# Kernel optimization log

Hardware: AMD Instinct MI355X
Metric: run time of the kernel (lower is better)

The kernel has to match this reference:

```python
import jax, jax.numpy as jnp
import numpy as np

B, L, H, V, HALF = 128, 4096, 64, 64, 32
ALPHA = 0.95
LN_EPS = 1e-5


def _normalize(x):
    # torch F.normalize(dim=-1): x / max(||x||_2, 1e-12)
    n = jnp.linalg.norm(x, axis=-1, keepdims=True)
    return x / jnp.maximum(n, 1e-12)


def setup_inputs() -> dict:
    key = jax.random.key(0)
    ks = jax.random.split(key, 17)
    s = 0.05
    return {
        "seq": jax.random.randint(ks[0], (B, L), 0, V),
        "embed": jax.random.normal(ks[1], (V, H), jnp.float32),
        "W1": jax.random.normal(ks[2], (H, 2 * H), jnp.float32) * s,
        "b1": jnp.zeros((2 * H,), jnp.float32),
        "W2": jax.random.normal(ks[3], (2 * H, H), jnp.float32) * s,
        "b2": jnp.zeros((H,), jnp.float32),
        "gamma": jnp.ones((H,), jnp.float32),
        "beta": jnp.zeros((H,), jnp.float32),
        "Ws": jax.random.normal(ks[4], (H, HALF), jnp.float32) * s,
        "bs": jnp.zeros((HALF,), jnp.float32),
        "We": jax.random.normal(ks[5], (H, HALF), jnp.float32) * s,
        "be": jnp.zeros((HALF,), jnp.float32),
        "Wrp": jax.random.normal(ks[6], (2 * HALF, H), jnp.float32) * s,
        "brp": jnp.zeros((H,), jnp.float32),
        "Wout": jax.random.normal(ks[7], (H, V), jnp.float32) * s,
        "bout": jnp.zeros((V,), jnp.float32),
    }


def _forward(seq, embed, W1, b1, W2, b2, gamma, beta,
             Ws, bs, We, be, Wrp, brp, Wout, bout):
    # Encoder: embed + FF(ReLU) residual + LayerNorm
    h0 = embed[seq]                                   # [B,L,H]
    ff = jnp.maximum(h0 @ W1 + b1, 0.0) @ W2 + b2
    x = h0 + ff
    mu = x.mean(-1, keepdims=True)
    var = ((x - mu) ** 2).mean(-1, keepdims=True)
    h = (x - mu) / jnp.sqrt(var + LN_EPS) * gamma + beta  # [B,L,H]

    # Precompute per-step projections for t = 0 .. L-2
    hp = h[:, :-1, :]                                 # [B,L-1,H]
    hs = hp @ Ws + bs                                 # [B,L-1,HALF]
    he = hp @ We + be
    ksn = _normalize(hs)
    ken = _normalize(he)
    scale = (jnp.arange(L - 1, dtype=h.dtype) + 1.0) / L  # (t+1)/L

    def step(carry, inp):
        M_s, M_e = carry                              # [B,HALF,HALF]
        hs_t, he_t, ks_t, ke_t, sc = inp
        vps = jnp.einsum('bij,bj->bi', M_s, ks_t)
        vpe = jnp.einsum('bij,bj->bi', M_e, ke_t)
        M_s = M_s + (1.0 - ALPHA) * (hs_t - vps)[:, :, None] * ks_t[:, None, :]
        M_e = M_e + (1.0 - ALPHA) * sc * (he_t - vpe)[:, :, None] * ke_t[:, None, :]
        return (M_s, M_e), None

    xs = (jnp.swapaxes(hs, 0, 1), jnp.swapaxes(he, 0, 1),
          jnp.swapaxes(ksn, 0, 1), jnp.swapaxes(ken, 0, 1), scale)
    M0 = jnp.zeros((B, HALF, HALF), h.dtype)
    (M_s, M_e), _ = jax.lax.scan(step, (M0, M0), xs)

    # Read with last-token query
    q = h[:, -1, :]
    qs = _normalize(q @ Ws + bs)
    qe = _normalize(q @ We + be)
    rs = jnp.einsum('bij,bj->bi', M_s, qs)
    re = jnp.einsum('bij,bj->bi', M_e, qe)
    r = jnp.concatenate([rs, re], axis=-1)            # [B,2*HALF]
    return (r @ Wrp + brp) @ Wout + bout              # [B,V]


def reference(seq, embed, W1, b1, W2, b2, gamma, beta,
              Ws, bs, We, be, Wrp, brp, Wout, bout):
    return _forward(seq, embed, W1, b1, W2, b2, gamma, beta,
                    Ws, bs, We, be, Wrp, brp, Wout, bout)
```

## Files before the change

kernel.cpp:

```cpp
#include <hip/hip_runtime.h>
#include <hip/hip_bf16.h>
#include <stdint.h>


#define BETA 0.05f
#define NB 128
#define NL 4096
#define TC 16
#define NCH 256
#define NBLD 6
#define SLOT_F 336
#define NSLOT 12

#define L_GR   (NSLOT * SLOT_F)
#define L_DA   (L_GR + 4096)
#define L_RV   (L_DA + 64)
#define L_O1   (L_RV + 64)
#define L_WHO  (L_O1 + 64)
#define L_TOT  (L_WHO + 1)

struct Ptrs { const void* p[15]; };

__device__ inline float readlane_f(float v, int l) {
    return __int_as_float(__builtin_amdgcn_readlane(__float_as_int(v), l));
}
__device__ inline float ldT(const float* p, int i) { return p[i]; }
__device__ inline float ldT(const __hip_bfloat16* p, int i) { return __bfloat162float(p[i]); }

template <typename T>
__device__ void build_tables_body(const T* emb, const T* W1, const T* b1,
                                  const T* W2, const T* b2, const T* gam,
                                  const T* bet, const T* Wsm, const T* bsv,
                                  const T* Wem, const T* bev, float* tbl)
{
    int v = blockIdx.x;
    int j = threadIdx.x;
    __shared__ float h0s[64];
    __shared__ float act[128];
    __shared__ float hrow[64];

    float h0 = ldT(emb, v * 64 + j);
    h0s[j] = h0;
    __syncthreads();

    float za = ldT(b1, j);
    float zb = ldT(b1, j + 64);
    for (int k = 0; k < 64; ++k) {
        float hk = h0s[k];
        za = fmaf(hk, ldT(W1, k * 128 + j), za);
        zb = fmaf(hk, ldT(W1, k * 128 + j + 64), zb);
    }
    act[j] = fmaxf(za, 0.0f);
    act[j + 64] = fmaxf(zb, 0.0f);
    __syncthreads();

    float ff = ldT(b2, j);
    for (int k = 0; k < 128; ++k)
        ff = fmaf(act[k], ldT(W2, k * 64 + j), ff);
    float x = h0 + ff;

    float s = x;
    for (int off = 32; off >= 1; off >>= 1) s += __shfl_xor(s, off, 64);
    float mu = s * (1.0f / 64.0f);
    float d = x - mu;
    float s2 = d * d;
    for (int off = 32; off >= 1; off >>= 1) s2 += __shfl_xor(s2, off, 64);
    float var = s2 * (1.0f / 64.0f);
    float h = d / sqrtf(var + 1e-5f) * ldT(gam, j) + ldT(bet, j);
    hrow[j] = h;
    __syncthreads();

    if (j < 32) {
        float sv = ldT(bsv, j);
        for (int k = 0; k < 64; ++k)
            sv = fmaf(hrow[k], ldT(Wsm, k * 32 + j), sv);
        float n2 = sv * sv;
        for (int off = 16; off >= 1; off >>= 1) n2 += __shfl_xor(n2, off, 64);
        float nrm = fmaxf(sqrtf(n2), 1e-12f);
        tbl[v * 32 + j] = sv;
        tbl[2048 + v * 32 + j] = sv / nrm;
    } else {
        int jj = j - 32;
        float ev = ldT(bev, jj);
        for (int k = 0; k < 64; ++k)
            ev = fmaf(hrow[k], ldT(Wem, k * 32 + jj), ev);
        float n2 = ev * ev;
        for (int off = 16; off >= 1; off >>= 1) n2 += __shfl_xor(n2, off, 64);
        float nrm = fmaxf(sqrtf(n2), 1e-12f);
        tbl[4096 + v * 32 + jj] = ev;
        tbl[6144 + v * 32 + jj] = ev / nrm;
    }
}

__global__ __launch_bounds__(64, 2) void build_tables(Ptrs ps, float* __restrict__ tbl,
                                                      int* __restrict__ flags)
{
    if (blockIdx.x == 0) {
        flags[threadIdx.x] = 0;
        flags[threadIdx.x + 64] = 0;
    }
    uint32_t g0 = *(const uint32_t*)ps.p[5];
    if (g0 == 0x3F803F80u)
        build_tables_body((const __hip_bfloat16*)ps.p[0], (const __hip_bfloat16*)ps.p[1],
                          (const __hip_bfloat16*)ps.p[2], (const __hip_bfloat16*)ps.p[3],
                          (const __hip_bfloat16*)ps.p[4], (const __hip_bfloat16*)ps.p[5],
                          (const __hip_bfloat16*)ps.p[6], (const __hip_bfloat16*)ps.p[7],
                          (const __hip_bfloat16*)ps.p[8], (const __hip_bfloat16*)ps.p[9],
                          (const __hip_bfloat16*)ps.p[10], tbl);
    else
        build_tables_body((const float*)ps.p[0], (const float*)ps.p[1],
                          (const float*)ps.p[2], (const float*)ps.p[3],
                          (const float*)ps.p[4], (const float*)ps.p[5],
                          (const float*)ps.p[6], (const float*)ps.p[7],
                          (const float*)ps.p[8], (const float*)ps.p[9],
                          (const float*)ps.p[10], tbl);
}

__global__ __launch_bounds__(512, 1) void ema_ms(
    const int* __restrict__ seq, const float* __restrict__ tbl,
    Ptrs ps, float* __restrict__ rvbuf, int* __restrict__ flags,
    void* __restrict__ outv)
{
    __shared__ __align__(16) float S[L_TOT];

    int bm = blockIdx.x;
    int b = bm >> 1, mat = bm & 1;
    int tid = threadIdx.x;
    int wid = tid >> 6, lane = tid & 63;
    const float bstep = BETA / 4096.0f;

    if (tid < 64) S[L_DA + tid] = 0.0f;

    const float* ktab = tbl + 2048 + mat * 4096;
    for (int i = tid; i < 2048; i += 512)
        S[(i >> 5) * 33 + (i & 31)] = ktab[i];
    __syncthreads();

    {
        float Kown[32];
#pragma unroll
        for (int j = 0; j < 32; ++j) Kown[j] = S[lane * 33 + j];
        for (int v8 = 0; v8 < 8; ++v8) {
            int vt = wid * 8 + v8;
            float acc = 0.0f;
#pragma unroll
            for (int j = 0; j < 32; ++j)
                acc = fmaf(S[vt * 33 + j], Kown[j], acc);
            S[L_GR + vt * 64 + lane] = acc;
        }
    }
    __syncthreads();

    const int* sb = seq + (size_t)b * NL;
    float y = 0.0f;
    if (wid == 0) {
        int vlast = sb[NL - 1];
        y = S[L_GR + vlast * 64 + lane];
    }

    const int NRND = (NCH + NBLD - 1) / NBLD;

    for (int r = 0; r <= NRND; ++r) {
        if (wid != 0 && wid != 4) {
            int bi = (wid > 4) ? (wid - 2) : (wid - 1);
            int ci = NBLD * r + bi;
            if (r < NRND && ci < NCH) {
                int c = NCH - 1 - ci;
                float* slot = S + ((r & 1) * NBLD + bi) * SLOT_F;
                int tokv = 0; float bneg = 0.0f;
                if (lane < TC) {
                    int t = c * TC + (TC - 1) - lane;
                    tokv = sb[t];
                    float bb = mat ? bstep * (float)(t + 1) : BETA;
                    if (t == NL - 1) bb = 0.0f;
                    bneg = -bb;
                    ((int*)(slot + 320))[lane] = tokv;
                }
                float garr[TC];
#pragma unroll
                for (int p = 0; p < TC; ++p) {
                    int vp = __builtin_amdgcn_readlane(tokv, p);
                    garr[p] = S[L_GR + vp * 64 + tokv] * bneg;
                }
                float z[TC];
                z[15] = (lane == 15) ? 1.0f : 0.0f;
#pragma unroll
                for (int q = TC - 2; q >= 0; --q) {
                    float zq = (lane == q) ? 1.0f : 0.0f;
#pragma unroll
                    for (int j2 = q + 1; j2 < TC; ++j2)
                        zq = fmaf(readlane_f(garr[j2], q), z[j2], zq);
                    z[q] = zq;
                }
                if (lane < TC) {
                    float4* vd = (float4*)(slot + lane * 20);
                    vd[0] = make_float4(z[0], z[1], z[2], z[3]);
                    vd[1] = make_float4(z[4], z[5], z[6], z[7]);
                    vd[2] = make_float4(z[8], z[9], z[10], z[11]);
                    vd[3] = make_float4(z[12], z[13], z[14], z[15]);
                }
            }
        } else if (wid == 0 && r >= 1) {
            int rpar = ((r - 1) & 1) * NBLD;
            int base_ci = NBLD * (r - 1);
            int nch_r = NCH - base_ci;
            if (nch_r > NBLD) nch_r = NBLD;
            int l15 = lane & 15;

            int tokr[NBLD];
#pragma unroll
            for (int j = 0; j < NBLD; ++j)
                tokr[j] = ((int*)(S + (rpar + j) * SLOT_F + 320))[l15];

            int stok[2][16];
            float gp[2][16];
            float4 V[2][4];
#pragma unroll
            for (int j = 0; j < 2; ++j) {
#pragma unroll
                for (int q = 0; q < 16; ++q)
                    stok[j][q] = __builtin_amdgcn_readlane(tokr[j], q);
                const float4* vr = (const float4*)(S + (rpar + j) * SLOT_F + l15 * 20);
#pragma unroll
                for (int k = 0; k < 4; ++k) V[j][k] = vr[k];
#pragma unroll
                for (int p = 0; p < 16; ++p)
                    gp[j][p] = S[L_GR + stok[j][p] * 64 + lane];
            }
            asm volatile("" ::: "memory");

#pragma unroll
            for (int jj = 0; jj < NBLD; ++jj) {
                const int pb = jj & 1;
                if (jj < nch_r) {
                    int c = NCH - 1 - (base_ci + jj);
                    float bv = 0.0f;
                    if (lane < TC) {
                        int t = c * TC + (TC - 1) - lane;
                        float bb = mat ? bstep * (float)(t + 1) : BETA;
                        if (t == NL - 1) bb = 0.0f;
                        bv = bb;
                    }
                    float ryq[16];
#pragma unroll
                    for (int q = 0; q < 16; ++q)
                        ryq[q] = readlane_f(y, stok[pb][q]);
                    float s0 = V[pb][0].x * ryq[0];
                    float s1 = V[pb][0].y * ryq[1];
                    float s2 = V[pb][0].z * ryq[2];
                    float s3 = V[pb][0].w * ryq[3];
                    s0 = fmaf(V[pb][1].x, ryq[4], s0);
                    s1 = fmaf(V[pb][1].y, ryq[5], s1);
                    s2 = fmaf(V[pb][1].z, ryq[6], s2);
                    s3 = fmaf(V[pb][1].w, ryq[7], s3);
                    s0 = fmaf(V[pb][2].x, ryq[8], s0);
                    s1 = fmaf(V[pb][2].y, ryq[9], s1);
                    s2 = fmaf(V[pb][2].z, ryq[10], s2);
                    s3 = fmaf(V[pb][2].w, ryq[11], s3);
                    s0 = fmaf(V[pb][3].x, ryq[12], s0);
                    s1 = fmaf(V[pb][3].y, ryq[13], s1);
                    s2 = fmaf(V[pb][3].z, ryq[14], s2);
                    s3 = fmaf(V[pb][3].w, ryq[15], s3);
                    float dv = ((s0 + s1) + (s2 + s3)) * bv;
                    float dn = -dv;
                    float ya = 0.f, yb = 0.f, yc2 = 0.f, yd = 0.f;
#pragma unroll
                    for (int p = 0; p < TC; p += 4) {
                        ya  = fmaf(readlane_f(dn, p),     gp[pb][p],     ya);
                        yb  = fmaf(readlane_f(dn, p + 1), gp[pb][p + 1], yb);
                        yc2 = fmaf(readlane_f(dn, p + 2), gp[pb][p + 2], yc2);
                        yd  = fmaf(readlane_f(dn, p + 3), gp[pb][p + 3], yd);
                    }
                    y += (ya + yb) + (yc2 + yd);
                    if (lane < TC) atomicAdd(&S[L_DA + tokr[jj]], dv);
                }
                if (jj + 2 < NBLD) {
                    const int j2 = jj + 2;
#pragma unroll
                    for (int q = 0; q < 16; ++q)
                        stok[pb][q] = __builtin_amdgcn_readlane(tokr[j2], q);
                    const float4* vr = (const float4*)(S + (rpar + j2) * SLOT_F + l15 * 20);
#pragma unroll
                    for (int k = 0; k < 4; ++k) V[pb][k] = vr[k];
#pragma unroll
                    for (int p = 0; p < 16; ++p)
                        gp[pb][p] = S[L_GR + stok[pb][p] * 64 + lane];
                }
                asm volatile("" ::: "memory");
            }
        }
        __syncthreads();
    }

    if (tid < 32) {
        float rr = 0.0f;
        const float* hsrc = tbl + mat * 4096;
        for (int v = 0; v < 64; ++v)
            rr = fmaf(S[L_DA + v], hsrc[v * 32 + tid], rr);
        __hip_atomic_store(&rvbuf[bm * 32 + tid], rr,
                           __ATOMIC_RELAXED, __HIP_MEMORY_SCOPE_AGENT);
    }
    __syncthreads();
    if (tid == 0) {
        int old = __hip_atomic_fetch_add(&flags[b], 1,
                                         __ATOMIC_ACQ_REL, __HIP_MEMORY_SCOPE_AGENT);
        ((int*)S)[L_WHO] = old;
    }
    __syncthreads();
    if (((int*)S)[L_WHO] != 1) return;

    if (tid < 64)
        S[L_RV + tid] = __hip_atomic_load(&rvbuf[b * 64 + tid],
                                          __ATOMIC_RELAXED, __HIP_MEMORY_SCOPE_AGENT);
    __syncthreads();

    uint32_t g0h = *(const uint32_t*)ps.p[5];
    int isbf = (g0h == 0x3F803F80u) ? 1 : 0;
    if (tid < 64) {
        float o;
        if (isbf) {
            const __hip_bfloat16* W = (const __hip_bfloat16*)ps.p[11];
            o = __bfloat162float(((const __hip_bfloat16*)ps.p[12])[tid]);
            for (int i = 0; i < 64; ++i)
                o = fmaf(S[L_RV + i], __bfloat162float(W[i * 64 + tid]), o);
        } else {
            const float* W = (const float*)ps.p[11];
            o = ((const float*)ps.p[12])[tid];
            for (int i = 0; i < 64; ++i)
                o = fmaf(S[L_RV + i], W[i * 64 + tid], o);
        }
        S[L_O1 + tid] = o;
    }
    __syncthreads();
    if (tid < 64) {
        float o2;
        if (isbf) {
            const __hip_bfloat16* W = (const __hip_bfloat16*)ps.p[13];
            o2 = __bfloat162float(((const __hip_bfloat16*)ps.p[14])[tid]);
            for (int i = 0; i < 64; ++i)
                o2 = fmaf(S[L_O1 + i], __bfloat162float(W[i * 64 + tid]), o2);
            ((__hip_bfloat16*)outv)[b * 64 + tid] = __float2bfloat16(o2);
        } else {
            const float* W = (const float*)ps.p[13];
            o2 = ((const float*)ps.p[14])[tid];
            for (int i = 0; i < 64; ++i)
                o2 = fmaf(S[L_O1 + i], W[i * 64 + tid], o2);
            ((float*)outv)[b * 64 + tid] = o2;
        }
    }
}

extern "C" void kernel_launch(void* const* d_in, const int* in_sizes, int n_in,
                              void* d_out, int out_size, void* d_ws, size_t ws_size,
                              hipStream_t stream) {
    const int* seq = (const int*)d_in[0];
    Ptrs ps;
    for (int i = 0; i < 15; ++i) ps.p[i] = d_in[i + 1];

    float* tbl = (float*)d_ws;
    float* rvbuf = tbl + 8192;
    int* flags = (int*)(rvbuf + 8192);

    build_tables<<<64, 64, 0, stream>>>(ps, tbl, flags);
    ema_ms<<<NB * 2, 512, 0, stream>>>(seq, tbl, ps, rvbuf, flags, d_out);
}
```

Measured before the change: 191.2 us.

## Build four chunk tables per builder wave and enlarge rounds to cut barriers

Each builder wave now packs four 16-lane groups, each solving one chunk's triangular system with a forward-substitution recast using width-16 shuffles. A round therefore covers 24 chunks instead of 6, and the slot buffer grows to 48. This reduces the number of block-wide barrier rounds and uses all 64 lanes of each builder wave instead of 16. In exchange it costs more LDS, more serial work per round for the consumer wave, and shuffle-based cross-lane reads in place of readlane.

```diff
diff --git a/kernel.cpp b/kernel.cpp
--- a/kernel.cpp
+++ b/kernel.cpp
@@ -9,8 +9,9 @@
 #define TC 16
 #define NCH 256
 #define NBLD 6
+#define RCH 24
 #define SLOT_F 336
-#define NSLOT 12
+#define NSLOT 48
 
 #define L_GR   (NSLOT * SLOT_F)
 #define L_DA   (L_GR + 4096)
@@ -158,58 +159,62 @@
         y = S[L_GR + vlast * 64 + lane];
     }
 
-    const int NRND = (NCH + NBLD - 1) / NBLD;
+    const int NRND = (NCH + RCH - 1) / RCH;
 
     for (int r = 0; r <= NRND; ++r) {
         if (wid != 0 && wid != 4) {
             int bi = (wid > 4) ? (wid - 2) : (wid - 1);
-            int ci = NBLD * r + bi;
-            if (r < NRND && ci < NCH) {
-                int c = NCH - 1 - ci;
-                float* slot = S + ((r & 1) * NBLD + bi) * SLOT_F;
-                int tokv = 0; float bneg = 0.0f;
-                if (lane < TC) {
-                    int t = c * TC + (TC - 1) - lane;
-                    tokv = sb[t];
-                    float bb = mat ? bstep * (float)(t + 1) : BETA;
-                    if (t == NL - 1) bb = 0.0f;
-                    bneg = -bb;
-                    ((int*)(slot + 320))[lane] = tokv;
-                }
+            if (r < NRND) {
+                int g = lane >> 4, q = lane & 15;
+                int ci = RCH * r + 4 * bi + g;
+                int valid = (ci < NCH);
+                int cic = valid ? ci : (NCH - 1);
+                int c = NCH - 1 - cic;
+                float* slot = S + ((r & 1) * RCH + 4 * bi + g) * SLOT_F;
+                int t = c * TC + (TC - 1) - q;
+                int tokv = sb[t];
+                float bb = mat ? bstep * (float)(t + 1) : BETA;
+                if (t == NL - 1) bb = 0.0f;
+                float bneg = -bb;
+                if (valid) ((int*)(slot + 320))[q] = tokv;
+
                 float garr[TC];
 #pragma unroll
                 for (int p = 0; p < TC; ++p) {
-                    int vp = __builtin_amdgcn_readlane(tokv, p);
+                    int vp = __shfl(tokv, p, 16);
                     garr[p] = S[L_GR + vp * 64 + tokv] * bneg;
                 }
-                float z[TC];
-                z[15] = (lane == 15) ? 1.0f : 0.0f;
-#pragma unroll
-                for (int q = TC - 2; q >= 0; --q) {
-                    float zq = (lane == q) ? 1.0f : 0.0f;
-#pragma unroll
-                    for (int j2 = q + 1; j2 < TC; ++j2)
-                        zq = fmaf(readlane_f(garr[j2], q), z[j2], zq);
-                    z[q] = zq;
-                }
-                if (lane < TC) {
-                    float4* vd = (float4*)(slot + lane * 20);
-                    vd[0] = make_float4(z[0], z[1], z[2], z[3]);
-                    vd[1] = make_float4(z[4], z[5], z[6], z[7]);
-                    vd[2] = make_float4(z[8], z[9], z[10], z[11]);
-                    vd[3] = make_float4(z[12], z[13], z[14], z[15]);
+                float x[TC];
+                x[0] = (q == 0) ? 1.0f : 0.0f;
+#pragma unroll
+                for (int p = 1; p < TC; ++p) {
+                    float t0 = 0.f, t1 = 0.f, t2 = 0.f, t3 = 0.f;
+#pragma unroll
+                    for (int j2 = 0; j2 < p; ++j2) {
+                        float cpj = __shfl(garr[p], j2, 16);
+                        if ((j2 & 3) == 0)      t0 = fmaf(cpj, x[j2], t0);
+                        else if ((j2 & 3) == 1) t1 = fmaf(cpj, x[j2], t1);
+                        else if ((j2 & 3) == 2) t2 = fmaf(cpj, x[j2], t2);
+                        else                    t3 = fmaf(cpj, x[j2], t3);
+                    }
+                    x[p] = ((q == p) ? 1.0f : 0.0f) + ((t0 + t1) + (t2 + t3));
+                }
+                if (valid) {
+#pragma unroll
+                    for (int p = 0; p < TC; ++p)
+                        slot[p * 20 + q] = x[p];
                 }
             }
         } else if (wid == 0 && r >= 1) {
-            int rpar = ((r - 1) & 1) * NBLD;
-            int base_ci = NBLD * (r - 1);
+            int rpar = ((r - 1) & 1) * RCH;
+            int base_ci = RCH * (r - 1);
             int nch_r = NCH - base_ci;
-            if (nch_r > NBLD) nch_r = NBLD;
+            if (nch_r > RCH) nch_r = RCH;
             int l15 = lane & 15;
 
-            int tokr[NBLD];
-#pragma unroll
-            for (int j = 0; j < NBLD; ++j)
+            int tokr[RCH];
+#pragma unroll
+            for (int j = 0; j < RCH; ++j)
                 tokr[j] = ((int*)(S + (rpar + j) * SLOT_F + 320))[l15];
 
             int stok[2][16];
@@ -230,7 +235,7 @@
             asm volatile("" ::: "memory");
 
 #pragma unroll
-            for (int jj = 0; jj < NBLD; ++jj) {
+            for (int jj = 0; jj < RCH; ++jj) {
                 const int pb = jj & 1;
                 if (jj < nch_r) {
                     int c = NCH - 1 - (base_ci + jj);
@@ -274,7 +279,7 @@
                     y += (ya + yb) + (yc2 + yd);
                     if (lane < TC) atomicAdd(&S[L_DA + tokr[jj]], dv);
                 }
-                if (jj + 2 < NBLD) {
+                if (jj + 2 < RCH) {
                     const int j2 = jj + 2;
 #pragma unroll
                     for (int q = 0; q < 16; ++q)
```

Result: no change. 189.0 us (-1.1%).

## Precompute per-chunk combined W matrix in builder waves to shorten serial scan

Applied to the files above, without the earlier changes.

Builder waves now do more per chunk. They compute the forward triangular solve with beta folded in, then precompute a 64x16 matrix W = X^T·(beta·G) and store it in enlarged LDS slots. The serial wave 0 no longer gathers G rows or runs the dependent readlane reduction over dv; it does two independent 16-term dot products per chunk, one for the y update and one for the accumulated delta. The sign is fixed at the end by negating rr. This moves work off the critical serial path in exchange for more LDS per slot and more builder-side arithmetic.

```diff
diff --git a/kernel.cpp b/kernel.cpp
--- a/kernel.cpp
+++ b/kernel.cpp
@@ -9,7 +9,7 @@
 #define TC 16
 #define NCH 256
 #define NBLD 6
-#define SLOT_F 336
+#define SLOT_F 1616
 #define NSLOT 12
 
 #define L_GR   (NSLOT * SLOT_F)
@@ -174,30 +174,57 @@
                     float bb = mat ? bstep * (float)(t + 1) : BETA;
                     if (t == NL - 1) bb = 0.0f;
                     bneg = -bb;
-                    ((int*)(slot + 320))[lane] = tokv;
-                }
-                float garr[TC];
+                    ((int*)(slot + 1600))[lane] = tokv;
+                }
+                float garr[TC], gp[TC];
 #pragma unroll
                 for (int p = 0; p < TC; ++p) {
                     int vp = __builtin_amdgcn_readlane(tokv, p);
                     garr[p] = S[L_GR + vp * 64 + tokv] * bneg;
-                }
-                float z[TC];
-                z[15] = (lane == 15) ? 1.0f : 0.0f;
-#pragma unroll
-                for (int q = TC - 2; q >= 0; --q) {
-                    float zq = (lane == q) ? 1.0f : 0.0f;
-#pragma unroll
-                    for (int j2 = q + 1; j2 < TC; ++j2)
-                        zq = fmaf(readlane_f(garr[j2], q), z[j2], zq);
-                    z[q] = zq;
+                    gp[p]   = S[L_GR + vp * 64 + lane];
+                }
+                float x[TC];
+                x[0] = (lane == 0) ? 1.0f : 0.0f;
+#pragma unroll
+                for (int p = 1; p < TC; ++p) {
+                    float t0 = 0.f, t1 = 0.f, t2 = 0.f, t3 = 0.f;
+#pragma unroll
+                    for (int j2 = 0; j2 < p; ++j2) {
+                        float cpj = readlane_f(garr[p], j2);
+                        if ((j2 & 3) == 0)      t0 = fmaf(cpj, x[j2], t0);
+                        else if ((j2 & 3) == 1) t1 = fmaf(cpj, x[j2], t1);
+                        else if ((j2 & 3) == 2) t2 = fmaf(cpj, x[j2], t2);
+                        else                    t3 = fmaf(cpj, x[j2], t3);
+                    }
+                    x[p] = ((lane == p) ? 1.0f : 0.0f) + ((t0 + t1) + (t2 + t3));
                 }
                 if (lane < TC) {
-                    float4* vd = (float4*)(slot + lane * 20);
-                    vd[0] = make_float4(z[0], z[1], z[2], z[3]);
-                    vd[1] = make_float4(z[4], z[5], z[6], z[7]);
-                    vd[2] = make_float4(z[8], z[9], z[10], z[11]);
-                    vd[3] = make_float4(z[12], z[13], z[14], z[15]);
+#pragma unroll
+                    for (int p = 0; p < TC; ++p)
+                        slot[p * 20 + lane] = x[p] * readlane_f(bneg, p);
+                }
+                float gpb[TC];
+#pragma unroll
+                for (int p = 0; p < TC; ++p)
+                    gpb[p] = gp[p] * readlane_f(bneg, p);
+                float4* wd = (float4*)(slot + 320 + lane * 20);
+#pragma unroll
+                for (int q4 = 0; q4 < 4; ++q4) {
+                    float w[4];
+#pragma unroll
+                    for (int qi = 0; qi < 4; ++qi) {
+                        const int q = 4 * q4 + qi;
+                        float a0 = 0.f, a1 = 0.f, a2 = 0.f, a3 = 0.f;
+#pragma unroll
+                        for (int p = 0; p < TC; p += 4) {
+                            a0 = fmaf(readlane_f(x[p],     q), gpb[p],     a0);
+                            a1 = fmaf(readlane_f(x[p + 1], q), gpb[p + 1], a1);
+                            a2 = fmaf(readlane_f(x[p + 2], q), gpb[p + 2], a2);
+                            a3 = fmaf(readlane_f(x[p + 3], q), gpb[p + 3], a3);
+                        }
+                        w[qi] = (a0 + a1) + (a2 + a3);
+                    }
+                    wd[q4] = make_float4(w[0], w[1], w[2], w[3]);
                 }
             }
         } else if (wid == 0 && r >= 1) {
@@ -210,22 +237,22 @@
             int tokr[NBLD];
 #pragma unroll
             for (int j = 0; j < NBLD; ++j)
-                tokr[j] = ((int*)(S + (rpar + j) * SLOT_F + 320))[l15];
+                tokr[j] = ((int*)(S + (rpar + j) * SLOT_F + 1600))[l15];
 
             int stok[2][16];
-            float gp[2][16];
-            float4 V[2][4];
+            float4 W4[2][4];
+            float4 V4[2][4];
 #pragma unroll
             for (int j = 0; j < 2; ++j) {
 #pragma unroll
                 for (int q = 0; q < 16; ++q)
                     stok[j][q] = __builtin_amdgcn_readlane(tokr[j], q);
+                const float4* wr = (const float4*)(S + (rpar + j) * SLOT_F + 320 + lane * 20);
+#pragma unroll
+                for (int k = 0; k < 4; ++k) W4[j][k] = wr[k];
                 const float4* vr = (const float4*)(S + (rpar + j) * SLOT_F + l15 * 20);
 #pragma unroll
-                for (int k = 0; k < 4; ++k) V[j][k] = vr[k];
-#pragma unroll
-                for (int p = 0; p < 16; ++p)
-                    gp[j][p] = S[L_GR + stok[j][p] * 64 + lane];
+                for (int k = 0; k < 4; ++k) V4[j][k] = vr[k];
             }
             asm volatile("" ::: "memory");
 
@@ -233,58 +260,47 @@
             for (int jj = 0; jj < NBLD; ++jj) {
                 const int pb = jj & 1;
                 if (jj < nch_r) {
-                    int c = NCH - 1 - (base_ci + jj);
-                    float bv = 0.0f;
-                    if (lane < TC) {
-                        int t = c * TC + (TC - 1) - lane;
-                        float bb = mat ? bstep * (float)(t + 1) : BETA;
-                        if (t == NL - 1) bb = 0.0f;
-                        bv = bb;
-                    }
                     float ryq[16];
 #pragma unroll
                     for (int q = 0; q < 16; ++q)
                         ryq[q] = readlane_f(y, stok[pb][q]);
-                    float s0 = V[pb][0].x * ryq[0];
-                    float s1 = V[pb][0].y * ryq[1];
-                    float s2 = V[pb][0].z * ryq[2];
-                    float s3 = V[pb][0].w * ryq[3];
-                    s0 = fmaf(V[pb][1].x, ryq[4], s0);
-                    s1 = fmaf(V[pb][1].y, ryq[5], s1);
-                    s2 = fmaf(V[pb][1].z, ryq[6], s2);
-                    s3 = fmaf(V[pb][1].w, ryq[7], s3);
-                    s0 = fmaf(V[pb][2].x, ryq[8], s0);
-                    s1 = fmaf(V[pb][2].y, ryq[9], s1);
-                    s2 = fmaf(V[pb][2].z, ryq[10], s2);
-                    s3 = fmaf(V[pb][2].w, ryq[11], s3);
-                    s0 = fmaf(V[pb][3].x, ryq[12], s0);
-                    s1 = fmaf(V[pb][3].y, ryq[13], s1);
-                    s2 = fmaf(V[pb][3].z, ryq[14], s2);
-                    s3 = fmaf(V[pb][3].w, ryq[15], s3);
-                    float dv = ((s0 + s1) + (s2 + s3)) * bv;
-                    float dn = -dv;
-                    float ya = 0.f, yb = 0.f, yc2 = 0.f, yd = 0.f;
-#pragma unroll
-                    for (int p = 0; p < TC; p += 4) {
-                        ya  = fmaf(readlane_f(dn, p),     gp[pb][p],     ya);
-                        yb  = fmaf(readlane_f(dn, p + 1), gp[pb][p + 1], yb);
-                        yc2 = fmaf(readlane_f(dn, p + 2), gp[pb][p + 2], yc2);
-                        yd  = fmaf(readlane_f(dn, p + 3), gp[pb][p + 3], yd);
+                    float ya = W4[pb][0].x * ryq[0];
+                    float yb = W4[pb][0].y * ryq[1];
+                    float yc2 = W4[pb][0].z * ryq[2];
+                    float yd = W4[pb][0].w * ryq[3];
+#pragma unroll
+                    for (int k = 1; k < 4; ++k) {
+                        ya  = fmaf(W4[pb][k].x, ryq[4 * k + 0], ya);
+                        yb  = fmaf(W4[pb][k].y, ryq[4 * k + 1], yb);
+                        yc2 = fmaf(W4[pb][k].z, ryq[4 * k + 2], yc2);
+                        yd  = fmaf(W4[pb][k].w, ryq[4 * k + 3], yd);
                     }
                     y += (ya + yb) + (yc2 + yd);
-                    if (lane < TC) atomicAdd(&S[L_DA + tokr[jj]], dv);
+                    float s0 = V4[pb][0].x * ryq[0];
+                    float s1 = V4[pb][0].y * ryq[1];
+                    float s2 = V4[pb][0].z * ryq[2];
+                    float s3 = V4[pb][0].w * ryq[3];
+#pragma unroll
+                    for (int k = 1; k < 4; ++k) {
+                        s0 = fmaf(V4[pb][k].x, ryq[4 * k + 0], s0);
+                        s1 = fmaf(V4[pb][k].y, ryq[4 * k + 1], s1);
+                        s2 = fmaf(V4[pb][k].z, ryq[4 * k + 2], s2);
+                        s3 = fmaf(V4[pb][k].w, ryq[4 * k + 3], s3);
+                    }
+                    float sp = (s0 + s1) + (s2 + s3);
+                    if (lane < TC) atomicAdd(&S[L_DA + tokr[jj]], sp);
                 }
                 if (jj + 2 < NBLD) {
                     const int j2 = jj + 2;
 #pragma unroll
                     for (int q = 0; q < 16; ++q)
                         stok[pb][q] = __builtin_amdgcn_readlane(tokr[j2], q);
+                    const float4* wr = (const float4*)(S + (rpar + j2) * SLOT_F + 320 + lane * 20);
+#pragma unroll
+                    for (int k = 0; k < 4; ++k) W4[pb][k] = wr[k];
                     const float4* vr = (const float4*)(S + (rpar + j2) * SLOT_F + l15 * 20);
 #pragma unroll
-                    for (int k = 0; k < 4; ++k) V[pb][k] = vr[k];
-#pragma unroll
-                    for (int p = 0; p < 16; ++p)
-                        gp[pb][p] = S[L_GR + stok[pb][p] * 64 + lane];
+                    for (int k = 0; k < 4; ++k) V4[pb][k] = vr[k];
                 }
                 asm volatile("" ::: "memory");
             }
@@ -297,7 +313,7 @@
         const float* hsrc = tbl + mat * 4096;
         for (int v = 0; v < 64; ++v)
             rr = fmaf(S[L_DA + v], hsrc[v * 32 + tid], rr);
-        __hip_atomic_store(&rvbuf[bm * 32 + tid], rr,
+        __hip_atomic_store(&rvbuf[bm * 32 + tid], -rr,
                            __ATOMIC_RELAXED, __HIP_MEMORY_SCOPE_AGENT);
     }
     __syncthreads();
```

New measurement: 258.1 us. 35.0% more time.
